# Optimization experiments

Hardware: AMD Instinct MI355X
Metric: run time of the kernel (lower is better)

## Reference

```python
import math
import jax, jax.numpy as jnp
import numpy as np

B, T, C, H = 4, 1024, 1024, 16
HD = C // H
BLOCK = 1024


def setup_inputs() -> dict:
    key = jax.random.key(0)
    k0, k1, k2, k3 = jax.random.split(key, 4)
    x = jax.random.normal(k0, (B, T, C), dtype=jnp.float32)
    # torch Linear weight is (out, in); we store (in, out) and apply x @ W + b
    W_attn = jax.random.normal(k1, (C, 3 * C), dtype=jnp.float32) * 0.02
    b_attn = jnp.zeros((3 * C,), dtype=jnp.float32)
    W_proj = jax.random.normal(k2, (C, C), dtype=jnp.float32) * 0.02
    b_proj = jnp.zeros((C,), dtype=jnp.float32)
    # rel_pos_emb: (n_head, block_size, head_dim), std 0.02 (leading 1 dim dropped)
    rel_pos_emb = jax.random.normal(k3, (H, BLOCK, HD), dtype=jnp.float32) * 0.02
    return {"x": x, "W_attn": W_attn, "b_attn": b_attn,
            "W_proj": W_proj, "b_proj": b_proj, "rel_pos_emb": rel_pos_emb}


def reference(x, W_attn, b_attn, W_proj, b_proj, rel_pos_emb):
    Bx, Tx, Cx = x.shape
    qkv = x @ W_attn + b_attn                      # (B, T, 3C)
    q, k, v = jnp.split(qkv, 3, axis=2)
    q = q.reshape(Bx, Tx, H, HD).transpose(0, 2, 1, 3)   # (B, H, T, hd)
    k = k.reshape(Bx, Tx, H, HD).transpose(0, 2, 1, 3)
    v = v.reshape(Bx, Tx, H, HD).transpose(0, 2, 1, 3)

    att = jnp.einsum('bhid,bhjd->bhij', q, k)      # (B, H, T, T)

    # relative position score: pos[b,h,i,j] = sum_d E[h, clamp(i-j,0), d] * k[b,h,j,d]
    # compute P[b,h,r,j] = <E[h,r,:], k[b,h,j,:]> then gather r = clamp(i-j, 0)
    rng = jnp.arange(Tx)
    dist = jnp.clip(rng[:, None] - rng[None, :], 0, None)          # (T, T)
    P = jnp.einsum('hrd,bhjd->bhrj', rel_pos_emb[:, :Tx], k)       # (B, H, T, T)
    pos_score = jnp.take_along_axis(P, dist[None, None, :, :], axis=2)
    att = att + pos_score

    att = att * (1.0 / math.sqrt(HD))
    causal = jnp.tril(jnp.ones((Tx, Tx), dtype=bool))
    att = jnp.where(causal[None, None], att, -jnp.inf)
    att = jax.nn.softmax(att, axis=-1)
    # dropout p=0.0 -> identity
    y = jnp.einsum('bhij,bhjd->bhid', att, v)      # (B, H, T, hd)
    y = y.transpose(0, 2, 1, 3).reshape(Bx, Tx, Cx)
    return y @ W_proj + b_proj
```

## Files before the change

### kernel.cpp

```cpp
#include <hip/hip_runtime.h>


typedef __bf16 bf16x8 __attribute__((ext_vector_type(8)));
typedef float f32x4 __attribute__((ext_vector_type(4)));
typedef unsigned short ushort_t;

#define T_SEQ 1024
#define NHEAD 16
#define HDIM 64
#define PLANE 4194304

__device__ __forceinline__ float bf2f(ushort_t h) {
    unsigned int u = ((unsigned int)h) << 16;
    float f; __builtin_memcpy(&f, &u, 4); return f;
}
__device__ __forceinline__ ushort_t f2bf(float f) {
    unsigned int u; __builtin_memcpy(&u, &f, 4);
    u = u + 0x7FFFu + ((u >> 16) & 1u);
    return (ushort_t)(u >> 16);
}

__global__ __launch_bounds__(256) void sentinel_kernel(float* out, int n, float val) {
    const int i = blockIdx.x * 256 + threadIdx.x;
    if (i < n) out[i] = val;
}

__global__ __launch_bounds__(256) void convert2(
    const float* __restrict__ x, ushort_t* __restrict__ x16,
    const float* __restrict__ E, ushort_t* __restrict__ E16)
{
    const int bid = blockIdx.x;
    const float* src; ushort_t* dst; int base;
    if (bid < 4096) { src = x; dst = x16; base = bid * 1024; }
    else            { src = E; dst = E16; base = (bid - 4096) * 1024; }
    const int i = base + (int)threadIdx.x * 4;
    const float4 v = *reinterpret_cast<const float4*>(src + i);
    union { unsigned long long u; ushort_t s[4]; } o;
    o.s[0] = f2bf(v.x); o.s[1] = f2bf(v.y); o.s[2] = f2bf(v.z); o.s[3] = f2bf(v.w);
    *reinterpret_cast<unsigned long long*>(dst + i) = o.u;
}

__global__ __launch_bounds__(256) void transpose_bf16(
    const float* __restrict__ W, ushort_t* __restrict__ Wt, int Kdim, int Ndim)
{
    __shared__ ushort_t t[64][65];
    const int n0 = blockIdx.x * 64, k0 = blockIdx.y * 64;
    const int cx = threadIdx.x & 63, ry = threadIdx.x >> 6;
#pragma unroll
    for (int i = 0; i < 16; i++) {
        const int r = ry + i * 4;
        t[r][cx] = f2bf(W[(size_t)(k0 + r) * Ndim + n0 + cx]);
    }
    __syncthreads();
#pragma unroll
    for (int i = 0; i < 16; i++) {
        const int r = ry + i * 4;
        Wt[(size_t)(n0 + r) * Kdim + k0 + cx] = t[cx][r];
    }
}

__global__ __launch_bounds__(256) void transpose_v(
    const ushort_t* __restrict__ v, ushort_t* __restrict__ vT)
{
    __shared__ ushort_t t[64][65];
    const int bh = blockIdx.y;
    const int t0 = blockIdx.x * 64;
    const int cx = threadIdx.x & 63, ry = threadIdx.x >> 6;
    const ushort_t* src = v + (size_t)bh * 65536;
    ushort_t* dst = vT + (size_t)bh * 65536;
#pragma unroll
    for (int i = 0; i < 16; i++) {
        const int r = ry + i * 4;
        t[r][cx] = src[(size_t)(t0 + r) * HDIM + cx];
    }
    __syncthreads();
#pragma unroll
    for (int i = 0; i < 16; i++) {
        const int d = ry + i * 4;
        dst[(size_t)d * T_SEQ + t0 + cx] = t[cx][d];
    }
}

template <int MODE>
__global__ __launch_bounds__(256) void gemm128(
    const ushort_t* __restrict__ A16, const ushort_t* __restrict__ Bt,
    const float* __restrict__ bias, void* __restrict__ out_,
    int Ndim, int Kdim)
{
    __shared__ __align__(16) ushort_t As[128 * 32];
    __shared__ __align__(16) ushort_t Bs[128 * 32];

    const int tid = threadIdx.x;
    const int w = tid >> 6;
    const int lane = tid & 63;
    const int l15 = lane & 15;
    const int quad = lane >> 4;
    const int m0 = blockIdx.y * 128, n0 = blockIdx.x * 128;
    const int wm = (w & 1) * 64, wn = (w >> 1) * 64;

    f32x4 acc[4][4];
#pragma unroll
    for (int mt = 0; mt < 4; mt++)
#pragma unroll
        for (int nt = 0; nt < 4; nt++) acc[mt][nt] = (f32x4){0.f, 0.f, 0.f, 0.f};

    for (int kk = 0; kk < Kdim; kk += 32) {
        __syncthreads();
#pragma unroll
        for (int t = 0; t < 2; t++) {
            const int chunk = w * 128 + t * 64 + lane;
            const int row = chunk >> 2, kc = (chunk & 3) * 8;
            __builtin_amdgcn_global_load_lds(
                (const __attribute__((address_space(1))) void*)
                    (A16 + (size_t)(m0 + row) * Kdim + kk + kc),
                (__attribute__((address_space(3))) void*)
                    (As + (size_t)(w * 128 + t * 64) * 8), 16, 0, 0);
            __builtin_amdgcn_global_load_lds(
                (const __attribute__((address_space(1))) void*)
                    (Bt + (size_t)(n0 + row) * Kdim + kk + kc),
                (__attribute__((address_space(3))) void*)
                    (Bs + (size_t)(w * 128 + t * 64) * 8), 16, 0, 0);
        }
        __syncthreads();

        bf16x8 af[4], bf[4];
#pragma unroll
        for (int mt = 0; mt < 4; mt++)
            af[mt] = *reinterpret_cast<const bf16x8*>(&As[(wm + mt * 16 + l15) * 32 + quad * 8]);
#pragma unroll
        for (int nt = 0; nt < 4; nt++)
            bf[nt] = *reinterpret_cast<const bf16x8*>(&Bs[(wn + nt * 16 + l15) * 32 + quad * 8]);
#pragma unroll
        for (int mt = 0; mt < 4; mt++)
#pragma unroll
            for (int nt = 0; nt < 4; nt++)
                acc[mt][nt] = __builtin_amdgcn_mfma_f32_16x16x32_bf16(
                    af[mt], bf[nt], acc[mt][nt], 0, 0, 0);
    }

#pragma unroll
    for (int mt = 0; mt < 4; mt++)
#pragma unroll
        for (int nt = 0; nt < 4; nt++) {
            const int n = n0 + wn + nt * 16 + l15;
            const float bv = bias[n];
#pragma unroll
            for (int r = 0; r < 4; r++) {
                const int m = m0 + wm + mt * 16 + quad * 4 + r;
                const float val = acc[mt][nt][r] + bv;
                if (MODE == 0) {
                    ushort_t* ws = (ushort_t*)out_;
                    const int which = n >> 10;
                    const size_t pl = (which == 2) ? 3 : which;
                    const int cc = n & 1023;
                    const int h = cc >> 6, d = cc & 63;
                    const int b = m >> 10, t = m & 1023;
                    ws[pl * PLANE + ((size_t)(b * NHEAD + h) * T_SEQ + t) * HDIM + d] = f2bf(val);
                } else {
                    ((float*)out_)[(size_t)m * Ndim + n] = val;
                }
            }
        }
}

__global__ __launch_bounds__(256) void flash_attn(
    const ushort_t* __restrict__ qp, const ushort_t* __restrict__ kp,
    const ushort_t* __restrict__ vTp, const ushort_t* __restrict__ E16,
    ushort_t* __restrict__ y16)
{
    __shared__ __align__(16) ushort_t Ks[64 * 72];
    __shared__ __align__(16) ushort_t Vt[64 * 72];
    __shared__ __align__(16) ushort_t Es[128 * 72];
    __shared__ __align__(16) ushort_t Ps[64 * 64 + 16];

    const int bh = blockIdx.y;
    const int h = bh & (NHEAD - 1);
    const int b = bh >> 4;
    const int tid = threadIdx.x;
    const int w = tid >> 6;
    const int lane = tid & 63;
    const int l15 = lane & 15;
    const int quad = lane >> 4;

    const size_t base = (size_t)bh * T_SEQ * HDIM;
    const ushort_t* Eh = E16 + (size_t)h * T_SEQ * HDIM;
    const ushort_t* vTb = vTp + (size_t)bh * 65536;
    const float c1 = 0.125f * 1.44269504f;

    const int rq = tid >> 2, cq = (tid & 3) * 16;
    const int re = tid >> 1, ce = (tid & 1) * 32;

    bf16x8 ones;
#pragma unroll
    for (int i = 0; i < 8; i++) ones[i] = (__bf16)1.0f;

#pragma unroll 1
    for (int ph = 0; ph < 2; ph++) {
        const int it = ph ? (int)blockIdx.x : 15 - (int)blockIdx.x;
        const int i0 = it * 64;

        bf16x8 qf[2];
        {
            const ushort_t* qrow = qp + base + (size_t)(i0 + w * 16 + l15) * HDIM;
            qf[0] = *reinterpret_cast<const bf16x8*>(qrow + quad * 8);
            qf[1] = *reinterpret_cast<const bf16x8*>(qrow + 32 + quad * 8);
        }

        f32x4 o[4], o5;
#pragma unroll
        for (int dt = 0; dt < 4; dt++) o[dt] = (f32x4){0.f, 0.f, 0.f, 0.f};
        o5 = (f32x4){0.f, 0.f, 0.f, 0.f};
        float mrow[4];
#pragma unroll
        for (int r = 0; r < 4; r++) mrow[r] = -3e38f;

        for (int j0 = 0; j0 <= i0; j0 += 64) {
            const int d0 = i0 - j0;
            __syncthreads();
            {
                const ushort_t* ksrc = kp + base + (size_t)(j0 + rq) * HDIM + cq;
                *reinterpret_cast<uint4*>(&Ks[rq * 72 + cq]) = *reinterpret_cast<const uint4*>(ksrc);
                *reinterpret_cast<uint4*>(&Ks[rq * 72 + cq + 8]) = *reinterpret_cast<const uint4*>(ksrc + 8);
                const ushort_t* vsrc = vTb + (size_t)rq * T_SEQ + j0 + cq;
                *reinterpret_cast<uint4*>(&Vt[rq * 72 + cq]) = *reinterpret_cast<const uint4*>(vsrc);
                *reinterpret_cast<uint4*>(&Vt[rq * 72 + cq + 8]) = *reinterpret_cast<const uint4*>(vsrc + 8);
            }
            {
                int g = d0 - 64 + re;
                g = g < 0 ? 0 : (g > 1023 ? 1023 : g);
                const ushort_t* esrc = Eh + (size_t)g * HDIM + ce;
#pragma unroll
                for (int q16 = 0; q16 < 4; q16++)
                    *reinterpret_cast<uint4*>(&Es[re * 72 + ce + q16 * 8]) =
                        *reinterpret_cast<const uint4*>(esrc + q16 * 8);
            }
            __syncthreads();

            f32x4 s[4], pb[2][4];
#pragma unroll
            for (int nt = 0; nt < 4; nt++) {
                s[nt] = (f32x4){0.f, 0.f, 0.f, 0.f};
                pb[0][nt] = (f32x4){0.f, 0.f, 0.f, 0.f};
                pb[1][nt] = (f32x4){0.f, 0.f, 0.f, 0.f};
            }
#pragma unroll
            for (int ks = 0; ks < 2; ks++) {
                const int ko = ks * 32 + quad * 8;
                const bf16x8 ae0 = *reinterpret_cast<const bf16x8*>(&Es[(w * 32 + l15) * 72 + ko]);
                const bf16x8 ae1 = *reinterpret_cast<const bf16x8*>(&Es[(w * 32 + 16 + l15) * 72 + ko]);
#pragma unroll
                for (int nt = 0; nt < 4; nt++) {
                    const bf16x8 bk = *reinterpret_cast<const bf16x8*>(&Ks[(nt * 16 + l15) * 72 + ko]);
                    s[nt] = __builtin_amdgcn_mfma_f32_16x16x32_bf16(qf[ks], bk, s[nt], 0, 0, 0);
                    pb[0][nt] = __builtin_amdgcn_mfma_f32_16x16x32_bf16(ae0, bk, pb[0][nt], 0, 0, 0);
                    pb[1][nt] = __builtin_amdgcn_mfma_f32_16x16x32_bf16(ae1, bk, pb[1][nt], 0, 0, 0);
                }
            }
#pragma unroll
            for (int mf = 0; mf < 2; mf++)
#pragma unroll
                for (int nt = 0; nt < 4; nt++) {
                    const int jl = nt * 16 + l15;
#pragma unroll
                    for (int r = 0; r < 4; r++) {
                        const int br = w * 32 + mf * 16 + quad * 4 + r;
                        const int il_t = br - 64 + jl;
                        const int addr = ((unsigned)il_t < 64u) ? il_t * 64 + jl : 4096;
                        Ps[addr] = f2bf(pb[mf][nt][r]);
                    }
                }
            __syncthreads();

            float pv[4][4], mnew[4];
#pragma unroll
            for (int r = 0; r < 4; r++) mnew[r] = mrow[r];
            const int il0 = w * 16 + quad * 4;
            if (j0 < i0) {
#pragma unroll
                for (int nt = 0; nt < 4; nt++) {
                    const int jl = nt * 16 + l15;
#pragma unroll
                    for (int r = 0; r < 4; r++) {
                        const float sv = (s[nt][r] + bf2f(Ps[(il0 + r) * 64 + jl])) * c1;
                        pv[nt][r] = sv;
                        mnew[r] = fmaxf(mnew[r], sv);
                    }
                }
            } else {
#pragma unroll
                for (int nt = 0; nt < 4; nt++) {
                    const int jl = nt * 16 + l15;
#pragma unroll
                    for (int r = 0; r < 4; r++) {
                        const int il = il0 + r;
                        float sv = (s[nt][r] + bf2f(Ps[il * 64 + jl])) * c1;
                        if (jl > il) sv = -3e38f;
                        pv[nt][r] = sv;
                        mnew[r] = fmaxf(mnew[r], sv);
                    }
                }
            }
#pragma unroll
            for (int r = 0; r < 4; r++)
#pragma unroll
                for (int off = 1; off < 16; off <<= 1)
                    mnew[r] = fmaxf(mnew[r], __shfl_xor(mnew[r], off, 64));
            float alpha[4];
#pragma unroll
            for (int r = 0; r < 4; r++) {
                alpha[r] = exp2f(mrow[r] - mnew[r]);
                mrow[r] = mnew[r];
            }
#pragma unroll
            for (int nt = 0; nt < 4; nt++)
#pragma unroll
                for (int r = 0; r < 4; r++)
                    pv[nt][r] = exp2f(pv[nt][r] - mnew[r]);
#pragma unroll
            for (int dt = 0; dt < 4; dt++)
#pragma unroll
                for (int r = 0; r < 4; r++) o[dt][r] *= alpha[r];
#pragma unroll
            for (int r = 0; r < 4; r++) o5[r] *= alpha[r];
#pragma unroll
            for (int nt = 0; nt < 4; nt++)
#pragma unroll
                for (int r = 0; r < 4; r++)
                    Es[(w * 16 + quad * 4 + r) * 72 + nt * 16 + l15] = f2bf(pv[nt][r]);
            __syncthreads();

#pragma unroll
            for (int ks = 0; ks < 2; ks++) {
                const int ko = ks * 32 + quad * 8;
                const bf16x8 ap = *reinterpret_cast<const bf16x8*>(&Es[(w * 16 + l15) * 72 + ko]);
#pragma unroll
                for (int dt = 0; dt < 4; dt++) {
                    const bf16x8 bv = *reinterpret_cast<const bf16x8*>(&Vt[(dt * 16 + l15) * 72 + ko]);
                    o[dt] = __builtin_amdgcn_mfma_f32_16x16x32_bf16(ap, bv, o[dt], 0, 0, 0);
                }
                o5 = __builtin_amdgcn_mfma_f32_16x16x32_bf16(ap, ones, o5, 0, 0, 0);
            }
        }

        float inv[4];
#pragma unroll
        for (int r = 0; r < 4; r++) inv[r] = 1.0f / o5[r];
#pragma unroll
        for (int dt = 0; dt < 4; dt++)
#pragma unroll
            for (int r = 0; r < 4; r++) {
                const int il = w * 16 + quad * 4 + r;
                const int d = dt * 16 + l15;
                y16[((size_t)(b * T_SEQ + i0 + il)) * 1024 + h * 64 + d] = f2bf(o[dt][r] * inv[r]);
            }
    }
}

extern "C" void kernel_launch(void* const* d_in, const int* in_sizes, int n_in,
                              void* d_out, int out_size, void* d_ws, size_t ws_size,
                              hipStream_t stream) {
    float* out = (float*)d_out;

    const void* x = nullptr; const void* Wa = nullptr; const void* ba = nullptr;
    const void* Wp = nullptr; const void* bp = nullptr; const void* E = nullptr;
    int anomaly = 0;
    if (n_in != 6) {
        anomaly = 2;
    } else {
        int c1M = 0;
        for (int i = 0; i < 6; i++) {
            const int s = in_sizes[i];
            if      (s == 4194304) x  = d_in[i];
            else if (s == 3145728) Wa = d_in[i];
            else if (s == 3072)    ba = d_in[i];
            else if (s == 1024)    bp = d_in[i];
            else if (s == 1048576) { if (c1M == 0) Wp = d_in[i]; else E = d_in[i]; c1M++; }
            else anomaly = 1;
        }
        if (!x || !Wa || !ba || !Wp || !bp || !E || c1M != 2) anomaly = 1;
    }
    if (!anomaly && out_size != 4194304) anomaly = 3;
    if (!anomaly && ws_size < (size_t)52428800) anomaly = 4;
    if (anomaly) {
        sentinel_kernel<<<(out_size + 255) / 256, 256, 0, stream>>>(out, out_size, 1000.0f * anomaly);
        return;
    }

    ushort_t* ws   = (ushort_t*)d_ws;
    ushort_t* qp   = ws;
    ushort_t* kp   = ws + (size_t)PLANE;
    ushort_t* vTp  = ws + (size_t)2 * PLANE;
    ushort_t* vtmp = ws + (size_t)3 * PLANE;
    ushort_t* y16  = vtmp;
    ushort_t* x16  = ws + (size_t)4 * PLANE;
    ushort_t* WaT  = ws + (size_t)5 * PLANE;
    ushort_t* WpT  = WaT + (size_t)3145728;
    ushort_t* E16  = WpT + (size_t)1048576;

    convert2<<<5120, 256, 0, stream>>>((const float*)x, x16, (const float*)E, E16);
    transpose_bf16<<<dim3(48, 16), 256, 0, stream>>>((const float*)Wa, WaT, 1024, 3072);
    transpose_bf16<<<dim3(16, 16), 256, 0, stream>>>((const float*)Wp, WpT, 1024, 1024);

    gemm128<0><<<dim3(24, 32), 256, 0, stream>>>(x16, WaT, (const float*)ba, (void*)ws, 3072, 1024);

    transpose_v<<<dim3(16, 64), 256, 0, stream>>>(vtmp, vTp);

    flash_attn<<<dim3(8, 64), 256, 0, stream>>>(qp, kp, vTp, E16, y16);

    gemm128<1><<<dim3(8, 32), 256, 0, stream>>>(y16, WpT, (const float*)bp, (void*)out, 1024, 1024);
}
```

Baseline: 223.0 us.

## Give each attention block one query tile, swizzle LDS, drop one barrier

The flash attention kernel no longer pairs a heavy and a light query tile in each block. It now launches one block per (batch-head, tile), ordered heaviest tile first, so the scheduler does the load balancing. It also pads the positional-score tile rows to 68, XOR-swizzles the E/probability tile in LDS to cut bank conflicts, and removes the barrier before the P·V step, since each wave only reads the rows it wrote. f2bf now uses the native bf16 conversion instead of manual rounding. The cost is more blocks, each with a shorter life, and a reliance on wave-local LDS ordering being correct.

Result: no change. 219.1 us (-1.8%).

```diff
diff --git a/kernel.cpp b/kernel.cpp
--- a/kernel.cpp
+++ b/kernel.cpp
@@ -15,9 +15,8 @@
     float f; __builtin_memcpy(&f, &u, 4); return f;
 }
 __device__ __forceinline__ ushort_t f2bf(float f) {
-    unsigned int u; __builtin_memcpy(&u, &f, 4);
-    u = u + 0x7FFFu + ((u >> 16) & 1u);
-    return (ushort_t)(u >> 16);
+    __bf16 h = (__bf16)f;
+    ushort_t u; __builtin_memcpy(&u, &h, 2); return u;
 }
 
 __global__ __launch_bounds__(256) void sentinel_kernel(float* out, int n, float val) {
@@ -154,8 +153,8 @@
                     const size_t pl = (which == 2) ? 3 : which;
                     const int cc = n & 1023;
                     const int h = cc >> 6, d = cc & 63;
-                    const int b = m >> 10, t = m & 1023;
-                    ws[pl * PLANE + ((size_t)(b * NHEAD + h) * T_SEQ + t) * HDIM + d] = f2bf(val);
+                    const int bb = m >> 10, t = m & 1023;
+                    ws[pl * PLANE + ((size_t)(bb * NHEAD + h) * T_SEQ + t) * HDIM + d] = f2bf(val);
                 } else {
                     ((float*)out_)[(size_t)m * Ndim + n] = val;
                 }
@@ -171,11 +170,12 @@
     __shared__ __align__(16) ushort_t Ks[64 * 72];
     __shared__ __align__(16) ushort_t Vt[64 * 72];
     __shared__ __align__(16) ushort_t Es[128 * 72];
-    __shared__ __align__(16) ushort_t Ps[64 * 64 + 16];
-
-    const int bh = blockIdx.y;
+    __shared__ __align__(16) ushort_t Ps[64 * 68 + 16];
+
+    const int bh = blockIdx.x;
     const int h = bh & (NHEAD - 1);
     const int b = bh >> 4;
+    const int it = 15 - (int)blockIdx.y;
     const int tid = threadIdx.x;
     const int w = tid >> 6;
     const int lane = tid & 63;
@@ -190,170 +190,170 @@
     const int rq = tid >> 2, cq = (tid & 3) * 16;
     const int re = tid >> 1, ce = (tid & 1) * 32;
 
+    const int kosz = ((l15 >> 3) & 1) << 3;
+    const int pswz = ((quad >> 1) & 1) << 3;
+    const int l15p = l15 ^ pswz;
+    const int eswz = ((re >> 3) & 1) << 3;
+
     bf16x8 ones;
 #pragma unroll
     for (int i = 0; i < 8; i++) ones[i] = (__bf16)1.0f;
 
-#pragma unroll 1
-    for (int ph = 0; ph < 2; ph++) {
-        const int it = ph ? (int)blockIdx.x : 15 - (int)blockIdx.x;
-        const int i0 = it * 64;
-
-        bf16x8 qf[2];
+    const int i0 = it * 64;
+
+    bf16x8 qf[2];
+    {
+        const ushort_t* qrow = qp + base + (size_t)(i0 + w * 16 + l15) * HDIM;
+        qf[0] = *reinterpret_cast<const bf16x8*>(qrow + quad * 8);
+        qf[1] = *reinterpret_cast<const bf16x8*>(qrow + 32 + quad * 8);
+    }
+
+    f32x4 o[4], o5;
+#pragma unroll
+    for (int dt = 0; dt < 4; dt++) o[dt] = (f32x4){0.f, 0.f, 0.f, 0.f};
+    o5 = (f32x4){0.f, 0.f, 0.f, 0.f};
+    float mrow[4];
+#pragma unroll
+    for (int r = 0; r < 4; r++) mrow[r] = -3e38f;
+
+    for (int j0 = 0; j0 <= i0; j0 += 64) {
+        const int d0 = i0 - j0;
+        __syncthreads();
         {
-            const ushort_t* qrow = qp + base + (size_t)(i0 + w * 16 + l15) * HDIM;
-            qf[0] = *reinterpret_cast<const bf16x8*>(qrow + quad * 8);
-            qf[1] = *reinterpret_cast<const bf16x8*>(qrow + 32 + quad * 8);
-        }
-
-        f32x4 o[4], o5;
-#pragma unroll
-        for (int dt = 0; dt < 4; dt++) o[dt] = (f32x4){0.f, 0.f, 0.f, 0.f};
-        o5 = (f32x4){0.f, 0.f, 0.f, 0.f};
-        float mrow[4];
-#pragma unroll
-        for (int r = 0; r < 4; r++) mrow[r] = -3e38f;
-
-        for (int j0 = 0; j0 <= i0; j0 += 64) {
-            const int d0 = i0 - j0;
-            __syncthreads();
-            {
-                const ushort_t* ksrc = kp + base + (size_t)(j0 + rq) * HDIM + cq;
-                *reinterpret_cast<uint4*>(&Ks[rq * 72 + cq]) = *reinterpret_cast<const uint4*>(ksrc);
-                *reinterpret_cast<uint4*>(&Ks[rq * 72 + cq + 8]) = *reinterpret_cast<const uint4*>(ksrc + 8);
-                const ushort_t* vsrc = vTb + (size_t)rq * T_SEQ + j0 + cq;
-                *reinterpret_cast<uint4*>(&Vt[rq * 72 + cq]) = *reinterpret_cast<const uint4*>(vsrc);
-                *reinterpret_cast<uint4*>(&Vt[rq * 72 + cq + 8]) = *reinterpret_cast<const uint4*>(vsrc + 8);
-            }
-            {
-                int g = d0 - 64 + re;
-                g = g < 0 ? 0 : (g > 1023 ? 1023 : g);
-                const ushort_t* esrc = Eh + (size_t)g * HDIM + ce;
-#pragma unroll
-                for (int q16 = 0; q16 < 4; q16++)
-                    *reinterpret_cast<uint4*>(&Es[re * 72 + ce + q16 * 8]) =
-                        *reinterpret_cast<const uint4*>(esrc + q16 * 8);
-            }
-            __syncthreads();
-
-            f32x4 s[4], pb[2][4];
+            const ushort_t* ksrc = kp + base + (size_t)(j0 + rq) * HDIM + cq;
+            *reinterpret_cast<uint4*>(&Ks[rq * 72 + cq]) = *reinterpret_cast<const uint4*>(ksrc);
+            *reinterpret_cast<uint4*>(&Ks[rq * 72 + cq + 8]) = *reinterpret_cast<const uint4*>(ksrc + 8);
+            const ushort_t* vsrc = vTb + (size_t)rq * T_SEQ + j0 + cq;
+            *reinterpret_cast<uint4*>(&Vt[rq * 72 + cq]) = *reinterpret_cast<const uint4*>(vsrc);
+            *reinterpret_cast<uint4*>(&Vt[rq * 72 + cq + 8]) = *reinterpret_cast<const uint4*>(vsrc + 8);
+        }
+        {
+            int g = d0 - 64 + re;
+            g = g < 0 ? 0 : (g > 1023 ? 1023 : g);
+            const ushort_t* esrc = Eh + (size_t)g * HDIM + ce;
+#pragma unroll
+            for (int q16 = 0; q16 < 4; q16++)
+                *reinterpret_cast<uint4*>(&Es[re * 72 + ce + ((q16 * 8) ^ eswz)]) =
+                    *reinterpret_cast<const uint4*>(esrc + q16 * 8);
+        }
+        __syncthreads();
+
+        f32x4 s[4], pb[2][4];
+#pragma unroll
+        for (int nt = 0; nt < 4; nt++) {
+            s[nt] = (f32x4){0.f, 0.f, 0.f, 0.f};
+            pb[0][nt] = (f32x4){0.f, 0.f, 0.f, 0.f};
+            pb[1][nt] = (f32x4){0.f, 0.f, 0.f, 0.f};
+        }
+#pragma unroll
+        for (int ks = 0; ks < 2; ks++) {
+            const int ko = ks * 32 + quad * 8;
+            const bf16x8 ae0 = *reinterpret_cast<const bf16x8*>(&Es[(w * 32 + l15) * 72 + (ko ^ kosz)]);
+            const bf16x8 ae1 = *reinterpret_cast<const bf16x8*>(&Es[(w * 32 + 16 + l15) * 72 + (ko ^ kosz)]);
 #pragma unroll
             for (int nt = 0; nt < 4; nt++) {
-                s[nt] = (f32x4){0.f, 0.f, 0.f, 0.f};
-                pb[0][nt] = (f32x4){0.f, 0.f, 0.f, 0.f};
-                pb[1][nt] = (f32x4){0.f, 0.f, 0.f, 0.f};
-            }
-#pragma unroll
-            for (int ks = 0; ks < 2; ks++) {
-                const int ko = ks * 32 + quad * 8;
-                const bf16x8 ae0 = *reinterpret_cast<const bf16x8*>(&Es[(w * 32 + l15) * 72 + ko]);
-                const bf16x8 ae1 = *reinterpret_cast<const bf16x8*>(&Es[(w * 32 + 16 + l15) * 72 + ko]);
-#pragma unroll
-                for (int nt = 0; nt < 4; nt++) {
-                    const bf16x8 bk = *reinterpret_cast<const bf16x8*>(&Ks[(nt * 16 + l15) * 72 + ko]);
-                    s[nt] = __builtin_amdgcn_mfma_f32_16x16x32_bf16(qf[ks], bk, s[nt], 0, 0, 0);
-                    pb[0][nt] = __builtin_amdgcn_mfma_f32_16x16x32_bf16(ae0, bk, pb[0][nt], 0, 0, 0);
-                    pb[1][nt] = __builtin_amdgcn_mfma_f32_16x16x32_bf16(ae1, bk, pb[1][nt], 0, 0, 0);
+                const bf16x8 bk = *reinterpret_cast<const bf16x8*>(&Ks[(nt * 16 + l15) * 72 + ko]);
+                s[nt] = __builtin_amdgcn_mfma_f32_16x16x32_bf16(qf[ks], bk, s[nt], 0, 0, 0);
+                pb[0][nt] = __builtin_amdgcn_mfma_f32_16x16x32_bf16(ae0, bk, pb[0][nt], 0, 0, 0);
+                pb[1][nt] = __builtin_amdgcn_mfma_f32_16x16x32_bf16(ae1, bk, pb[1][nt], 0, 0, 0);
+            }
+        }
+#pragma unroll
+        for (int mf = 0; mf < 2; mf++)
+#pragma unroll
+            for (int nt = 0; nt < 4; nt++) {
+                const int jl = nt * 16 + l15;
+#pragma unroll
+                for (int r = 0; r < 4; r++) {
+                    const int br = w * 32 + mf * 16 + quad * 4 + r;
+                    const int il_t = br - 64 + jl;
+                    const int addr = ((unsigned)il_t < 64u) ? il_t * 68 + jl : 4352;
+                    Ps[addr] = f2bf(pb[mf][nt][r]);
                 }
             }
-#pragma unroll
-            for (int mf = 0; mf < 2; mf++)
-#pragma unroll
-                for (int nt = 0; nt < 4; nt++) {
-                    const int jl = nt * 16 + l15;
-#pragma unroll
-                    for (int r = 0; r < 4; r++) {
-                        const int br = w * 32 + mf * 16 + quad * 4 + r;
-                        const int il_t = br - 64 + jl;
-                        const int addr = ((unsigned)il_t < 64u) ? il_t * 64 + jl : 4096;
-                        Ps[addr] = f2bf(pb[mf][nt][r]);
-                    }
+        __syncthreads();
+
+        float pv[4][4], mnew[4];
+#pragma unroll
+        for (int r = 0; r < 4; r++) mnew[r] = mrow[r];
+        const int il0 = w * 16 + quad * 4;
+        if (j0 < i0) {
+#pragma unroll
+            for (int nt = 0; nt < 4; nt++) {
+                const int jl = nt * 16 + l15;
+#pragma unroll
+                for (int r = 0; r < 4; r++) {
+                    const float sv = (s[nt][r] + bf2f(Ps[(il0 + r) * 68 + jl])) * c1;
+                    pv[nt][r] = sv;
+                    mnew[r] = fmaxf(mnew[r], sv);
                 }
-            __syncthreads();
-
-            float pv[4][4], mnew[4];
-#pragma unroll
-            for (int r = 0; r < 4; r++) mnew[r] = mrow[r];
-            const int il0 = w * 16 + quad * 4;
-            if (j0 < i0) {
-#pragma unroll
-                for (int nt = 0; nt < 4; nt++) {
-                    const int jl = nt * 16 + l15;
-#pragma unroll
-                    for (int r = 0; r < 4; r++) {
-                        const float sv = (s[nt][r] + bf2f(Ps[(il0 + r) * 64 + jl])) * c1;
-                        pv[nt][r] = sv;
-                        mnew[r] = fmaxf(mnew[r], sv);
-                    }
+            }
+        } else {
+#pragma unroll
+            for (int nt = 0; nt < 4; nt++) {
+                const int jl = nt * 16 + l15;
+#pragma unroll
+                for (int r = 0; r < 4; r++) {
+                    const int il = il0 + r;
+                    float sv = (s[nt][r] + bf2f(Ps[il * 68 + jl])) * c1;
+                    if (jl > il) sv = -3e38f;
+                    pv[nt][r] = sv;
+                    mnew[r] = fmaxf(mnew[r], sv);
                 }
-            } else {
-#pragma unroll
-                for (int nt = 0; nt < 4; nt++) {
-                    const int jl = nt * 16 + l15;
-#pragma unroll
-                    for (int r = 0; r < 4; r++) {
-                        const int il = il0 + r;
-                        float sv = (s[nt][r] + bf2f(Ps[il * 64 + jl])) * c1;
-                        if (jl > il) sv = -3e38f;
-                        pv[nt][r] = sv;
-                        mnew[r] = fmaxf(mnew[r], sv);
-                    }
-                }
-            }
+            }
+        }
+#pragma unroll
+        for (int r = 0; r < 4; r++)
+#pragma unroll
+            for (int off = 1; off < 16; off <<= 1)
+                mnew[r] = fmaxf(mnew[r], __shfl_xor(mnew[r], off, 64));
+        float alpha[4];
+#pragma unroll
+        for (int r = 0; r < 4; r++) {
+            alpha[r] = exp2f(mrow[r] - mnew[r]);
+            mrow[r] = mnew[r];
+        }
+#pragma unroll
+        for (int nt = 0; nt < 4; nt++)
 #pragma unroll
             for (int r = 0; r < 4; r++)
-#pragma unroll
-                for (int off = 1; off < 16; off <<= 1)
-                    mnew[r] = fmaxf(mnew[r], __shfl_xor(mnew[r], off, 64));
-            float alpha[4];
-#pragma unroll
-            for (int r = 0; r < 4; r++) {
-                alpha[r] = exp2f(mrow[r] - mnew[r]);
-                mrow[r] = mnew[r];
-            }
-#pragma unroll
-            for (int nt = 0; nt < 4; nt++)
-#pragma unroll
-                for (int r = 0; r < 4; r++)
-                    pv[nt][r] = exp2f(pv[nt][r] - mnew[r]);
-#pragma unroll
-            for (int dt = 0; dt < 4; dt++)
-#pragma unroll
-                for (int r = 0; r < 4; r++) o[dt][r] *= alpha[r];
-#pragma unroll
-            for (int r = 0; r < 4; r++) o5[r] *= alpha[r];
-#pragma unroll
-            for (int nt = 0; nt < 4; nt++)
-#pragma unroll
-                for (int r = 0; r < 4; r++)
-                    Es[(w * 16 + quad * 4 + r) * 72 + nt * 16 + l15] = f2bf(pv[nt][r]);
-            __syncthreads();
-
-#pragma unroll
-            for (int ks = 0; ks < 2; ks++) {
-                const int ko = ks * 32 + quad * 8;
-                const bf16x8 ap = *reinterpret_cast<const bf16x8*>(&Es[(w * 16 + l15) * 72 + ko]);
-#pragma unroll
-                for (int dt = 0; dt < 4; dt++) {
-                    const bf16x8 bv = *reinterpret_cast<const bf16x8*>(&Vt[(dt * 16 + l15) * 72 + ko]);
-                    o[dt] = __builtin_amdgcn_mfma_f32_16x16x32_bf16(ap, bv, o[dt], 0, 0, 0);
-                }
-                o5 = __builtin_amdgcn_mfma_f32_16x16x32_bf16(ap, ones, o5, 0, 0, 0);
-            }
-        }
-
-        float inv[4];
-#pragma unroll
-        for (int r = 0; r < 4; r++) inv[r] = 1.0f / o5[r];
+                pv[nt][r] = exp2f(pv[nt][r] - mnew[r]);
 #pragma unroll
         for (int dt = 0; dt < 4; dt++)
 #pragma unroll
-            for (int r = 0; r < 4; r++) {
-                const int il = w * 16 + quad * 4 + r;
-                const int d = dt * 16 + l15;
-                y16[((size_t)(b * T_SEQ + i0 + il)) * 1024 + h * 64 + d] = f2bf(o[dt][r] * inv[r]);
-            }
-    }
+            for (int r = 0; r < 4; r++) o[dt][r] *= alpha[r];
+#pragma unroll
+        for (int r = 0; r < 4; r++) o5[r] *= alpha[r];
+#pragma unroll
+        for (int nt = 0; nt < 4; nt++)
+#pragma unroll
+            for (int r = 0; r < 4; r++)
+                Es[(w * 16 + quad * 4 + r) * 72 + nt * 16 + l15p] = f2bf(pv[nt][r]);
+
+#pragma unroll
+        for (int ks = 0; ks < 2; ks++) {
+            const int ko = ks * 32 + quad * 8;
+            const bf16x8 ap = *reinterpret_cast<const bf16x8*>(&Es[(w * 16 + l15) * 72 + (ko ^ kosz)]);
+#pragma unroll
+            for (int dt = 0; dt < 4; dt++) {
+                const bf16x8 bv = *reinterpret_cast<const bf16x8*>(&Vt[(dt * 16 + l15) * 72 + ko]);
+                o[dt] = __builtin_amdgcn_mfma_f32_16x16x32_bf16(ap, bv, o[dt], 0, 0, 0);
+            }
+            o5 = __builtin_amdgcn_mfma_f32_16x16x32_bf16(ap, ones, o5, 0, 0, 0);
+        }
+    }
+
+    float inv[4];
+#pragma unroll
+    for (int r = 0; r < 4; r++) inv[r] = 1.0f / o5[r];
+#pragma unroll
+    for (int dt = 0; dt < 4; dt++)
+#pragma unroll
+        for (int r = 0; r < 4; r++) {
+            const int il = w * 16 + quad * 4 + r;
+            const int d = dt * 16 + l15;
+            y16[((size_t)(b * T_SEQ + i0 + il)) * 1024 + h * 64 + d] = f2bf(o[dt][r] * inv[r]);
+        }
 }
 
 extern "C" void kernel_launch(void* const* d_in, const int* in_sizes, int n_in,
@@ -405,7 +405,7 @@
 
     transpose_v<<<dim3(16, 64), 256, 0, stream>>>(vtmp, vTp);
 
-    flash_attn<<<dim3(8, 64), 256, 0, stream>>>(qp, kp, vTp, E16, y16);
+    flash_attn<<<dim3(64, 16), 256, 0, stream>>>(qp, kp, vTp, E16, y16);
 
     gemm128<1><<<dim3(8, 32), 256, 0, stream>>>(y16, WpT, (const float*)bp, (void*)out, 1024, 1024);
 }
```
